# Optimization experiments

Hardware: AMD Instinct MI355X
Metric: run time of the kernel (lower is better)

The kernel has to match this reference:

```python
import jax, jax.numpy as jnp
import numpy as np

NUM_EXPERTS = 16
HIDDEN = 1024
INTERMEDIATE = 4096
TOTAL_TOKENS = 32768  # 2048 tokens per expert


def setup_inputs() -> dict:
    key = jax.random.key(0)
    k1, k2, k3 = jax.random.split(key, 3)
    hidden_states = jax.random.normal(k1, (TOTAL_TOKENS, HIDDEN), dtype=jnp.float32)
    gate_up_proj = jax.random.normal(k2, (NUM_EXPERTS, HIDDEN, 2 * INTERMEDIATE), dtype=jnp.float32)
    down_proj = jax.random.normal(k3, (NUM_EXPERTS, INTERMEDIATE, HIDDEN), dtype=jnp.float32)
    return {"hidden_states": hidden_states, "gate_up_proj": gate_up_proj, "down_proj": down_proj}


def reference(hidden_states, gate_up_proj, down_proj):
    E, H = gate_up_proj.shape[0], gate_up_proj.shape[1]
    # (E, T, H): tokens pre-grouped by expert, as in the torch module's reshape
    x = hidden_states.reshape(E, -1, H)
    # batched expert GEMM: (E,T,H) @ (E,H,2I) -> (E,T,2I)
    gate_up = jnp.einsum('eth,ehf->etf', x, gate_up_proj)
    gate, up = jnp.split(gate_up, 2, axis=-1)
    gated = up * jax.nn.silu(gate)  # SwiGLU
    # down projection: (E,T,I) @ (E,I,H) -> (E,T,H)
    out = jnp.einsum('eti,eih->eth', gated, down_proj)
    return out.reshape(-1, H)
```

## Files before the change

### kernel.cpp

```cpp
#include <hip/hip_runtime.h>
#include <hip/hip_bf16.h>
#include <cstdint>
#include <cstddef>

#define NE  16
#define HD  1024
#define ID  4096
#define TPE 2048
#define TOKENS 32768

typedef __attribute__((ext_vector_type(8))) short short8;
typedef __attribute__((ext_vector_type(4))) float f32x4;
typedef __attribute__((ext_vector_type(4))) unsigned short u16x4;
typedef __attribute__((ext_vector_type(8))) unsigned short u16x8;

static __device__ __forceinline__ unsigned short f2b(float f) {
    __bf16 h = (__bf16)f;
    return __builtin_bit_cast(unsigned short, h);
}

#define GLOAD16(gsrc, ldsbase)                                                  \
    __builtin_amdgcn_global_load_lds(                                           \
        (const __attribute__((address_space(1))) unsigned int*)(gsrc),          \
        (__attribute__((address_space(3))) unsigned int*)(ldsbase), 16, 0, 0)

#define MFMA16(a, b, c) __builtin_amdgcn_mfma_f32_16x16x32_bf16((a), (b), (c), 0, 0, 0)

__global__ void k_f2b(const float* __restrict__ src, unsigned short* __restrict__ dst, int n4)
{
    int i = blockIdx.x * blockDim.x + threadIdx.x;
    int stride = gridDim.x * blockDim.x;
    for (; i < n4; i += stride) {
        float4 v = *(const float4*)(src + (size_t)i * 4);
        u16x4 b = { f2b(v.x), f2b(v.y), f2b(v.z), f2b(v.w) };
        *(u16x4*)(dst + (size_t)i * 4) = b;
    }
}

__global__ __launch_bounds__(256) void k_transpose(const float* __restrict__ src,
                                                   unsigned short* __restrict__ dst,
                                                   int K, int N, int e0)
{
    __shared__ unsigned short LT[64][72];
    const int t  = threadIdx.x;
    const int eL = blockIdx.z;
    const float* s = src + (size_t)(e0 + eL) * K * N
                         + (size_t)(blockIdx.y * 64) * N + blockIdx.x * 64;
    unsigned short* d = dst + (size_t)eL * N * K
                            + (size_t)(blockIdx.x * 64) * K + blockIdx.y * 64;
    #pragma unroll
    for (int i = 0; i < 4; ++i) {
        int row = i * 16 + (t >> 4);
        int c4  = (t & 15) * 4;
        float4 v = *(const float4*)(s + (size_t)row * N + c4);
        LT[c4 + 0][row] = f2b(v.x);
        LT[c4 + 1][row] = f2b(v.y);
        LT[c4 + 2][row] = f2b(v.z);
        LT[c4 + 3][row] = f2b(v.w);
    }
    __syncthreads();
    #pragma unroll
    for (int i = 0; i < 2; ++i) {
        int n  = i * 32 + (t >> 3);
        int k8 = (t & 7) * 8;
        u16x8 v = *(const u16x8*)&LT[n][k8];
        *(u16x8*)(d + (size_t)n * K + k8) = v;
    }
}

__global__ __launch_bounds__(512, 2) void k_gemm1(const unsigned short* __restrict__ hsB,
                                                  const unsigned short* __restrict__ gupT,
                                                  unsigned short* __restrict__ gated,
                                                  int e0)
{
    __shared__ unsigned short As[2][256 * 64];
    __shared__ unsigned short Bs[2][256 * 64];
    const int NT = HD / 64;

    const int t    = threadIdx.x;
    const int lane = t & 63;
    const int w    = t >> 6;
    const int wr   = w >> 2;
    const int wc   = w & 3;
    const int eL   = blockIdx.z;
    const int e    = e0 + eL;
    const int n0g  = blockIdx.x * 128;
    const int m0   = blockIdx.y * 256;

    const unsigned short* gA  = hsB  + (size_t)(e * TPE + m0) * HD;
    const unsigned short* gBt = gupT + (size_t)eL * (2 * ID) * HD;

    f32x4 acc[8][4];
    #pragma unroll
    for (int i = 0; i < 8; ++i)
        #pragma unroll
        for (int j = 0; j < 4; ++j)
            acc[i][j] = f32x4{0.f, 0.f, 0.f, 0.f};

    auto STAGE = [&](int buf, int kt) {
        #pragma unroll
        for (int i = 0; i < 4; ++i) {
            int idx = i * 512 + t;
            int row = idx >> 3, sl = idx & 7;
            GLOAD16(gA + (size_t)row * HD + kt * 64 + ((sl ^ (row & 7)) << 3),
                    &As[buf][(size_t)(i * 512 + (t & ~63)) * 8]);
        }
        #pragma unroll
        for (int i = 0; i < 4; ++i) {
            int idx = i * 512 + t;
            int c = idx >> 3, sl = idx & 7;
            int g = c >> 5, j = c & 31;
            int grow = ((g & 1) ? ID : 0) + n0g + ((g >> 1) << 5) + j;
            GLOAD16(gBt + (size_t)grow * HD + kt * 64 + ((sl ^ (c & 7)) << 3),
                    &Bs[buf][(size_t)(i * 512 + (t & ~63)) * 8]);
        }
    };

    STAGE(0, 0);
    STAGE(1, 1);
    asm volatile("s_waitcnt vmcnt(8)" ::: "memory");
    __builtin_amdgcn_s_barrier();

    for (int kt = 0; kt < NT; ++kt) {
        const int cur = kt & 1;
        const unsigned short* Ab = &As[cur][0];
        const unsigned short* Bb = &Bs[cur][0];

        short8 av[8], bv[4];
        #pragma unroll
        for (int fm = 0; fm < 8; ++fm) {
            int row = wr * 128 + fm * 16 + (lane & 15);
            int sl  = (lane >> 4);
            av[fm] = *(const short8*)&Ab[row * 64 + ((sl ^ (row & 7)) << 3)];
        }
        #pragma unroll
        for (int fn = 0; fn < 4; ++fn) {
            int c  = wc * 64 + fn * 16 + (lane & 15);
            int sl = (lane >> 4);
            bv[fn] = *(const short8*)&Bb[c * 64 + ((sl ^ (c & 7)) << 3)];
        }
        __builtin_amdgcn_s_setprio(1);
        #pragma unroll
        for (int fm = 0; fm < 8; ++fm)
            #pragma unroll
            for (int fn = 0; fn < 4; ++fn)
                acc[fm][fn] = MFMA16(av[fm], bv[fn], acc[fm][fn]);
        __builtin_amdgcn_s_setprio(0);

        short8 av1[8], bv1[4];
        #pragma unroll
        for (int fm = 0; fm < 8; ++fm) {
            int row = wr * 128 + fm * 16 + (lane & 15);
            int sl  = 4 + (lane >> 4);
            av1[fm] = *(const short8*)&Ab[row * 64 + ((sl ^ (row & 7)) << 3)];
        }
        #pragma unroll
        for (int fn = 0; fn < 4; ++fn) {
            int c  = wc * 64 + fn * 16 + (lane & 15);
            int sl = 4 + (lane >> 4);
            bv1[fn] = *(const short8*)&Bb[c * 64 + ((sl ^ (c & 7)) << 3)];
        }
        asm volatile("s_waitcnt lgkmcnt(0)" ::: "memory");
        __builtin_amdgcn_sched_barrier(0);
        __builtin_amdgcn_s_barrier();
        if (kt + 2 < NT) {
            STAGE(cur, kt + 2);
            asm volatile("s_waitcnt vmcnt(8)" ::: "memory");
        } else {
            asm volatile("s_waitcnt vmcnt(0)" ::: "memory");
        }
        __builtin_amdgcn_s_barrier();
        __builtin_amdgcn_s_setprio(1);
        #pragma unroll
        for (int fm = 0; fm < 8; ++fm)
            #pragma unroll
            for (int fn = 0; fn < 4; ++fn)
                acc[fm][fn] = MFMA16(av1[fm], bv1[fn], acc[fm][fn]);
        __builtin_amdgcn_s_setprio(0);
    }

    unsigned short* g0 = gated + ((size_t)eL * TPE + m0) * ID;
    const int rq = (lane >> 4) << 2;
    const int cl = lane & 15;
    #pragma unroll
    for (int fm = 0; fm < 8; ++fm) {
        #pragma unroll
        for (int fp = 0; fp < 2; ++fp) {
            f32x4 g = acc[fm][fp];
            f32x4 u = acc[fm][fp + 2];
            #pragma unroll
            for (int r = 0; r < 4; ++r) {
                float gv  = g[r];
                float val = u[r] * gv / (1.0f + __expf(-gv));
                int row = wr * 128 + fm * 16 + rq + r;
                int col = n0g + wc * 32 + fp * 16 + cl;
                g0[(size_t)row * ID + col] = f2b(val);
            }
        }
    }
}

__global__ __launch_bounds__(512, 2) void k_gemm2(const unsigned short* __restrict__ gated,
                                                  const unsigned short* __restrict__ dwnT,
                                                  float* __restrict__ out,
                                                  int e0)
{
    __shared__ unsigned short As[2][256 * 64];
    __shared__ unsigned short Bs[2][256 * 64];
    const int NT = ID / 64;

    const int t    = threadIdx.x;
    const int lane = t & 63;
    const int w    = t >> 6;
    const int wr   = w >> 2;
    const int wc   = w & 3;
    const int eL   = blockIdx.z;
    const int e    = e0 + eL;
    const int n0   = blockIdx.x * 256;
    const int m0   = blockIdx.y * 256;

    const unsigned short* gA  = gated + ((size_t)eL * TPE + m0) * ID;
    const unsigned short* gBt = dwnT  + (size_t)eL * HD * ID;

    f32x4 acc[8][4];
    #pragma unroll
    for (int i = 0; i < 8; ++i)
        #pragma unroll
        for (int j = 0; j < 4; ++j)
            acc[i][j] = f32x4{0.f, 0.f, 0.f, 0.f};

    auto STAGE = [&](int buf, int kt) {
        #pragma unroll
        for (int i = 0; i < 4; ++i) {
            int idx = i * 512 + t;
            int row = idx >> 3, sl = idx & 7;
            GLOAD16(gA + (size_t)row * ID + kt * 64 + ((sl ^ (row & 7)) << 3),
                    &As[buf][(size_t)(i * 512 + (t & ~63)) * 8]);
        }
        #pragma unroll
        for (int i = 0; i < 4; ++i) {
            int idx = i * 512 + t;
            int c = idx >> 3, sl = idx & 7;
            GLOAD16(gBt + (size_t)(n0 + c) * ID + kt * 64 + ((sl ^ (c & 7)) << 3),
                    &Bs[buf][(size_t)(i * 512 + (t & ~63)) * 8]);
        }
    };

    STAGE(0, 0);
    STAGE(1, 1);
    asm volatile("s_waitcnt vmcnt(8)" ::: "memory");
    __builtin_amdgcn_s_barrier();

    for (int kt = 0; kt < NT; ++kt) {
        const int cur = kt & 1;
        const unsigned short* Ab = &As[cur][0];
        const unsigned short* Bb = &Bs[cur][0];

        short8 av[8], bv[4];
        #pragma unroll
        for (int fm = 0; fm < 8; ++fm) {
            int row = wr * 128 + fm * 16 + (lane & 15);
            int sl  = (lane >> 4);
            av[fm] = *(const short8*)&Ab[row * 64 + ((sl ^ (row & 7)) << 3)];
        }
        #pragma unroll
        for (int fn = 0; fn < 4; ++fn) {
            int c  = wc * 64 + fn * 16 + (lane & 15);
            int sl = (lane >> 4);
            bv[fn] = *(const short8*)&Bb[c * 64 + ((sl ^ (c & 7)) << 3)];
        }
        __builtin_amdgcn_s_setprio(1);
        #pragma unroll
        for (int fm = 0; fm < 8; ++fm)
            #pragma unroll
            for (int fn = 0; fn < 4; ++fn)
                acc[fm][fn] = MFMA16(av[fm], bv[fn], acc[fm][fn]);
        __builtin_amdgcn_s_setprio(0);

        short8 av1[8], bv1[4];
        #pragma unroll
        for (int fm = 0; fm < 8; ++fm) {
            int row = wr * 128 + fm * 16 + (lane & 15);
            int sl  = 4 + (lane >> 4);
            av1[fm] = *(const short8*)&Ab[row * 64 + ((sl ^ (row & 7)) << 3)];
        }
        #pragma unroll
        for (int fn = 0; fn < 4; ++fn) {
            int c  = wc * 64 + fn * 16 + (lane & 15);
            int sl = 4 + (lane >> 4);
            bv1[fn] = *(const short8*)&Bb[c * 64 + ((sl ^ (c & 7)) << 3)];
        }
        asm volatile("s_waitcnt lgkmcnt(0)" ::: "memory");
        __builtin_amdgcn_sched_barrier(0);
        __builtin_amdgcn_s_barrier();
        if (kt + 2 < NT) {
            STAGE(cur, kt + 2);
            asm volatile("s_waitcnt vmcnt(8)" ::: "memory");
        } else {
            asm volatile("s_waitcnt vmcnt(0)" ::: "memory");
        }
        __builtin_amdgcn_s_barrier();
        __builtin_amdgcn_s_setprio(1);
        #pragma unroll
        for (int fm = 0; fm < 8; ++fm)
            #pragma unroll
            for (int fn = 0; fn < 4; ++fn)
                acc[fm][fn] = MFMA16(av1[fm], bv1[fn], acc[fm][fn]);
        __builtin_amdgcn_s_setprio(0);
    }

    float* o0 = out + (size_t)(e * TPE + m0) * HD;
    const int rq = (lane >> 4) << 2;
    const int cl = lane & 15;
    #pragma unroll
    for (int fm = 0; fm < 8; ++fm) {
        #pragma unroll
        for (int fn = 0; fn < 4; ++fn) {
            #pragma unroll
            for (int r = 0; r < 4; ++r) {
                int row = wr * 128 + fm * 16 + rq + r;
                int col = n0 + wc * 64 + fn * 16 + cl;
                o0[(size_t)row * HD + col] = acc[fm][fn][r];
            }
        }
    }
}

extern "C" void kernel_launch(void* const* d_in, const int* in_sizes, int n_in,
                              void* d_out, int out_size, void* d_ws, size_t ws_size,
                              hipStream_t stream)
{
    (void)in_sizes; (void)n_in; (void)out_size;
    const float* hs  = (const float*)d_in[0];
    const float* gup = (const float*)d_in[1];
    const float* dwn = (const float*)d_in[2];
    float* out = (float*)d_out;

    const size_t SZ_HSB   = (size_t)TOKENS * HD * 2;
    const size_t SZ_GUPT  = (size_t)2 * ID * HD * 2;
    const size_t SZ_DWNT  = (size_t)HD * ID * 2;
    const size_t SZ_GATED = (size_t)TPE * ID * 2;
    const size_t perExp   = SZ_GUPT + SZ_DWNT + SZ_GATED;

    int G = (ws_size > SZ_HSB) ? (int)((ws_size - SZ_HSB) / perExp) : 1;
    if (G < 1) G = 1;
    if (G > NE) G = NE;

    unsigned short* hsB   = (unsigned short*)d_ws;
    unsigned short* gupT  = (unsigned short*)((char*)d_ws + SZ_HSB);
    unsigned short* dwnT  = (unsigned short*)((char*)d_ws + SZ_HSB + (size_t)G * SZ_GUPT);
    unsigned short* gated = (unsigned short*)((char*)d_ws + SZ_HSB + (size_t)G * (SZ_GUPT + SZ_DWNT));

    k_f2b<<<2048, 256, 0, stream>>>(hs, hsB, TOKENS * HD / 4);

    for (int e0 = 0; e0 < NE; e0 += G) {
        int ne = NE - e0;
        if (ne > G) ne = G;
        k_transpose<<<dim3((2 * ID) / 64, HD / 64, ne), 256, 0, stream>>>(gup, gupT, HD, 2 * ID, e0);
        k_transpose<<<dim3(HD / 64, ID / 64, ne), 256, 0, stream>>>(dwn, dwnT, ID, HD, e0);
        k_gemm1<<<dim3(ID / 128, TPE / 256, ne), 512, 0, stream>>>(hsB, gupT, gated, e0);
        k_gemm2<<<dim3(HD / 256, TPE / 256, ne), 512, 0, stream>>>(gated, dwnT, out, e0);
    }
}
```

Measured before the change: 1.173 ms.

## Interleave split global-to-LDS staging with quarter-tile MFMA phases in both GEMMs

```diff
diff --git a/kernel.cpp b/kernel.cpp
--- a/kernel.cpp
+++ b/kernel.cpp
@@ -97,87 +97,133 @@
         for (int j = 0; j < 4; ++j)
             acc[i][j] = f32x4{0.f, 0.f, 0.f, 0.f};
 
-    auto STAGE = [&](int buf, int kt) {
-        #pragma unroll
-        for (int i = 0; i < 4; ++i) {
-            int idx = i * 512 + t;
-            int row = idx >> 3, sl = idx & 7;
+    auto stageA = [&](int buf, int kt, int fmh) {
+        #pragma unroll
+        for (int i = 0; i < 2; ++i) {
+            int r0  = fmh * 64 + w * 8 + i * 128;
+            int row = r0 + (lane >> 3);
+            int sl  = lane & 7;
             GLOAD16(gA + (size_t)row * HD + kt * 64 + ((sl ^ (row & 7)) << 3),
-                    &As[buf][(size_t)(i * 512 + (t & ~63)) * 8]);
-        }
-        #pragma unroll
-        for (int i = 0; i < 4; ++i) {
-            int idx = i * 512 + t;
-            int c = idx >> 3, sl = idx & 7;
-            int g = c >> 5, j = c & 31;
-            int grow = ((g & 1) ? ID : 0) + n0g + ((g >> 1) << 5) + j;
+                    &As[buf][r0 * 64]);
+        }
+    };
+    auto stageB = [&](int buf, int kt, int half) {
+        #pragma unroll
+        for (int i = 0; i < 2; ++i) {
+            int c0 = half * 128 + w * 8 + i * 64;
+            int c  = c0 + (lane >> 3);
+            int sl = lane & 7;
+            int g  = c >> 5;
+            int grow = ((g & 1) ? ID : 0) + n0g + ((g >> 1) << 5) + (c & 31);
             GLOAD16(gBt + (size_t)grow * HD + kt * 64 + ((sl ^ (c & 7)) << 3),
-                    &Bs[buf][(size_t)(i * 512 + (t & ~63)) * 8]);
+                    &Bs[buf][c0 * 64]);
         }
     };
 
-    STAGE(0, 0);
-    STAGE(1, 1);
+    stageA(0, 0, 0);  stageB(0, 0, 0);  stageB(0, 0, 1);
+    stageA(0, 0, 1);
+    stageA(1, 1, 0);  stageB(1, 1, 0);  stageB(1, 1, 1);
     asm volatile("s_waitcnt vmcnt(8)" ::: "memory");
     __builtin_amdgcn_s_barrier();
 
     for (int kt = 0; kt < NT; ++kt) {
-        const int cur = kt & 1;
+        const int cur = kt & 1, nxt = cur ^ 1;
         const unsigned short* Ab = &As[cur][0];
         const unsigned short* Bb = &Bs[cur][0];
-
-        short8 av[8], bv[4];
-        #pragma unroll
-        for (int fm = 0; fm < 8; ++fm) {
-            int row = wr * 128 + fm * 16 + (lane & 15);
-            int sl  = (lane >> 4);
-            av[fm] = *(const short8*)&Ab[row * 64 + ((sl ^ (row & 7)) << 3)];
-        }
-        #pragma unroll
-        for (int fn = 0; fn < 4; ++fn) {
-            int c  = wc * 64 + fn * 16 + (lane & 15);
-            int sl = (lane >> 4);
-            bv[fn] = *(const short8*)&Bb[c * 64 + ((sl ^ (c & 7)) << 3)];
-        }
-        __builtin_amdgcn_s_setprio(1);
-        #pragma unroll
-        for (int fm = 0; fm < 8; ++fm)
-            #pragma unroll
-            for (int fn = 0; fn < 4; ++fn)
-                acc[fm][fn] = MFMA16(av[fm], bv[fn], acc[fm][fn]);
-        __builtin_amdgcn_s_setprio(0);
-
-        short8 av1[8], bv1[4];
-        #pragma unroll
-        for (int fm = 0; fm < 8; ++fm) {
-            int row = wr * 128 + fm * 16 + (lane & 15);
-            int sl  = 4 + (lane >> 4);
-            av1[fm] = *(const short8*)&Ab[row * 64 + ((sl ^ (row & 7)) << 3)];
-        }
-        #pragma unroll
-        for (int fn = 0; fn < 4; ++fn) {
-            int c  = wc * 64 + fn * 16 + (lane & 15);
-            int sl = 4 + (lane >> 4);
-            bv1[fn] = *(const short8*)&Bb[c * 64 + ((sl ^ (c & 7)) << 3)];
-        }
-        asm volatile("s_waitcnt lgkmcnt(0)" ::: "memory");
-        __builtin_amdgcn_sched_barrier(0);
-        __builtin_amdgcn_s_barrier();
-        if (kt + 2 < NT) {
-            STAGE(cur, kt + 2);
-            asm volatile("s_waitcnt vmcnt(8)" ::: "memory");
-        } else {
-            asm volatile("s_waitcnt vmcnt(0)" ::: "memory");
-        }
-        __builtin_amdgcn_s_barrier();
-        __builtin_amdgcn_s_setprio(1);
-        #pragma unroll
-        for (int fm = 0; fm < 8; ++fm)
-            #pragma unroll
-            for (int fn = 0; fn < 4; ++fn)
-                acc[fm][fn] = MFMA16(av1[fm], bv1[fn], acc[fm][fn]);
-        __builtin_amdgcn_s_setprio(0);
-    }
+        const int ktn  = (kt + 1 < NT) ? kt + 1 : NT - 1;
+        const int ktn2 = (kt + 2 < NT) ? kt + 2 : NT - 1;
+
+        short8 av[8], bv[8];
+
+        stageA(nxt, ktn, 1);
+        #pragma unroll
+        for (int f = 0; f < 4; ++f)
+            #pragma unroll
+            for (int ks = 0; ks < 2; ++ks) {
+                int row = wr * 128 + f * 16 + (lane & 15);
+                int sl  = ks * 4 + (lane >> 4);
+                av[f * 2 + ks] = *(const short8*)&Ab[row * 64 + ((sl ^ (row & 7)) << 3)];
+            }
+        #pragma unroll
+        for (int fn = 0; fn < 2; ++fn)
+            #pragma unroll
+            for (int ks = 0; ks < 2; ++ks) {
+                int c  = wc * 64 + fn * 16 + (lane & 15);
+                int sl = ks * 4 + (lane >> 4);
+                bv[fn * 2 + ks] = *(const short8*)&Bb[c * 64 + ((sl ^ (c & 7)) << 3)];
+            }
+        asm volatile("s_waitcnt lgkmcnt(0)" ::: "memory");
+        __builtin_amdgcn_sched_barrier(0);
+        __builtin_amdgcn_s_setprio(1);
+        #pragma unroll
+        for (int f = 0; f < 4; ++f)
+            #pragma unroll
+            for (int fn = 0; fn < 2; ++fn)
+                #pragma unroll
+                for (int ks = 0; ks < 2; ++ks)
+                    acc[f][fn] = MFMA16(av[f * 2 + ks], bv[fn * 2 + ks], acc[f][fn]);
+        __builtin_amdgcn_s_setprio(0);
+        __builtin_amdgcn_s_barrier();
+
+        stageA(cur, ktn2, 0);
+        #pragma unroll
+        for (int fn = 2; fn < 4; ++fn)
+            #pragma unroll
+            for (int ks = 0; ks < 2; ++ks) {
+                int c  = wc * 64 + fn * 16 + (lane & 15);
+                int sl = ks * 4 + (lane >> 4);
+                bv[fn * 2 + ks] = *(const short8*)&Bb[c * 64 + ((sl ^ (c & 7)) << 3)];
+            }
+        asm volatile("s_waitcnt lgkmcnt(0)" ::: "memory");
+        __builtin_amdgcn_sched_barrier(0);
+        __builtin_amdgcn_s_setprio(1);
+        #pragma unroll
+        for (int f = 0; f < 4; ++f)
+            #pragma unroll
+            for (int fn = 2; fn < 4; ++fn)
+                #pragma unroll
+                for (int ks = 0; ks < 2; ++ks)
+                    acc[f][fn] = MFMA16(av[f * 2 + ks], bv[fn * 2 + ks], acc[f][fn]);
+        __builtin_amdgcn_s_setprio(0);
+        asm volatile("s_waitcnt vmcnt(10)" ::: "memory");
+        __builtin_amdgcn_s_barrier();
+
+        stageB(cur, ktn2, 0);
+        #pragma unroll
+        for (int f = 0; f < 4; ++f)
+            #pragma unroll
+            for (int ks = 0; ks < 2; ++ks) {
+                int row = wr * 128 + 64 + f * 16 + (lane & 15);
+                int sl  = ks * 4 + (lane >> 4);
+                av[f * 2 + ks] = *(const short8*)&Ab[row * 64 + ((sl ^ (row & 7)) << 3)];
+            }
+        asm volatile("s_waitcnt lgkmcnt(0)" ::: "memory");
+        __builtin_amdgcn_sched_barrier(0);
+        __builtin_amdgcn_s_setprio(1);
+        #pragma unroll
+        for (int f = 0; f < 4; ++f)
+            #pragma unroll
+            for (int fn = 0; fn < 2; ++fn)
+                #pragma unroll
+                for (int ks = 0; ks < 2; ++ks)
+                    acc[4 + f][fn] = MFMA16(av[f * 2 + ks], bv[fn * 2 + ks], acc[4 + f][fn]);
+        __builtin_amdgcn_s_setprio(0);
+        __builtin_amdgcn_s_barrier();
+
+        stageB(cur, ktn2, 1);
+        __builtin_amdgcn_s_setprio(1);
+        #pragma unroll
+        for (int f = 0; f < 4; ++f)
+            #pragma unroll
+            for (int fn = 2; fn < 4; ++fn)
+                #pragma unroll
+                for (int ks = 0; ks < 2; ++ks)
+                    acc[4 + f][fn] = MFMA16(av[f * 2 + ks], bv[fn * 2 + ks], acc[4 + f][fn]);
+        __builtin_amdgcn_s_setprio(0);
+        asm volatile("s_waitcnt vmcnt(8)" ::: "memory");
+        __builtin_amdgcn_s_barrier();
+    }
+    asm volatile("s_waitcnt vmcnt(0)" ::: "memory");
 
     unsigned short* g0 = gated + ((size_t)eL * TPE + m0) * ID;
     const int rq = (lane >> 4) << 2;
@@ -229,85 +275,131 @@
         for (int j = 0; j < 4; ++j)
             acc[i][j] = f32x4{0.f, 0.f, 0.f, 0.f};
 
-    auto STAGE = [&](int buf, int kt) {
-        #pragma unroll
-        for (int i = 0; i < 4; ++i) {
-            int idx = i * 512 + t;
-            int row = idx >> 3, sl = idx & 7;
+    auto stageA = [&](int buf, int kt, int fmh) {
+        #pragma unroll
+        for (int i = 0; i < 2; ++i) {
+            int r0  = fmh * 64 + w * 8 + i * 128;
+            int row = r0 + (lane >> 3);
+            int sl  = lane & 7;
             GLOAD16(gA + (size_t)row * ID + kt * 64 + ((sl ^ (row & 7)) << 3),
-                    &As[buf][(size_t)(i * 512 + (t & ~63)) * 8]);
-        }
-        #pragma unroll
-        for (int i = 0; i < 4; ++i) {
-            int idx = i * 512 + t;
-            int c = idx >> 3, sl = idx & 7;
+                    &As[buf][r0 * 64]);
+        }
+    };
+    auto stageB = [&](int buf, int kt, int half) {
+        #pragma unroll
+        for (int i = 0; i < 2; ++i) {
+            int c0 = half * 128 + w * 8 + i * 64;
+            int c  = c0 + (lane >> 3);
+            int sl = lane & 7;
             GLOAD16(gBt + (size_t)(n0 + c) * ID + kt * 64 + ((sl ^ (c & 7)) << 3),
-                    &Bs[buf][(size_t)(i * 512 + (t & ~63)) * 8]);
+                    &Bs[buf][c0 * 64]);
         }
     };
 
-    STAGE(0, 0);
-    STAGE(1, 1);
+    stageA(0, 0, 0);  stageB(0, 0, 0);  stageB(0, 0, 1);
+    stageA(0, 0, 1);
+    stageA(1, 1, 0);  stageB(1, 1, 0);  stageB(1, 1, 1);
     asm volatile("s_waitcnt vmcnt(8)" ::: "memory");
     __builtin_amdgcn_s_barrier();
 
     for (int kt = 0; kt < NT; ++kt) {
-        const int cur = kt & 1;
+        const int cur = kt & 1, nxt = cur ^ 1;
         const unsigned short* Ab = &As[cur][0];
         const unsigned short* Bb = &Bs[cur][0];
-
-        short8 av[8], bv[4];
-        #pragma unroll
-        for (int fm = 0; fm < 8; ++fm) {
-            int row = wr * 128 + fm * 16 + (lane & 15);
-            int sl  = (lane >> 4);
-            av[fm] = *(const short8*)&Ab[row * 64 + ((sl ^ (row & 7)) << 3)];
-        }
-        #pragma unroll
-        for (int fn = 0; fn < 4; ++fn) {
-            int c  = wc * 64 + fn * 16 + (lane & 15);
-            int sl = (lane >> 4);
-            bv[fn] = *(const short8*)&Bb[c * 64 + ((sl ^ (c & 7)) << 3)];
-        }
-        __builtin_amdgcn_s_setprio(1);
-        #pragma unroll
-        for (int fm = 0; fm < 8; ++fm)
-            #pragma unroll
-            for (int fn = 0; fn < 4; ++fn)
-                acc[fm][fn] = MFMA16(av[fm], bv[fn], acc[fm][fn]);
-        __builtin_amdgcn_s_setprio(0);
-
-        short8 av1[8], bv1[4];
-        #pragma unroll
-        for (int fm = 0; fm < 8; ++fm) {
-            int row = wr * 128 + fm * 16 + (lane & 15);
-            int sl  = 4 + (lane >> 4);
-            av1[fm] = *(const short8*)&Ab[row * 64 + ((sl ^ (row & 7)) << 3)];
-        }
-        #pragma unroll
-        for (int fn = 0; fn < 4; ++fn) {
-            int c  = wc * 64 + fn * 16 + (lane & 15);
-            int sl = 4 + (lane >> 4);
-            bv1[fn] = *(const short8*)&Bb[c * 64 + ((sl ^ (c & 7)) << 3)];
-        }
-        asm volatile("s_waitcnt lgkmcnt(0)" ::: "memory");
-        __builtin_amdgcn_sched_barrier(0);
-        __builtin_amdgcn_s_barrier();
-        if (kt + 2 < NT) {
-            STAGE(cur, kt + 2);
-            asm volatile("s_waitcnt vmcnt(8)" ::: "memory");
-        } else {
-            asm volatile("s_waitcnt vmcnt(0)" ::: "memory");
-        }
-        __builtin_amdgcn_s_barrier();
-        __builtin_amdgcn_s_setprio(1);
-        #pragma unroll
-        for (int fm = 0; fm < 8; ++fm)
-            #pragma unroll
-            for (int fn = 0; fn < 4; ++fn)
-                acc[fm][fn] = MFMA16(av1[fm], bv1[fn], acc[fm][fn]);
-        __builtin_amdgcn_s_setprio(0);
-    }
+        const int ktn  = (kt + 1 < NT) ? kt + 1 : NT - 1;
+        const int ktn2 = (kt + 2 < NT) ? kt + 2 : NT - 1;
+
+        short8 av[8], bv[8];
+
+        stageA(nxt, ktn, 1);
+        #pragma unroll
+        for (int f = 0; f < 4; ++f)
+            #pragma unroll
+            for (int ks = 0; ks < 2; ++ks) {
+                int row = wr * 128 + f * 16 + (lane & 15);
+                int sl  = ks * 4 + (lane >> 4);
+                av[f * 2 + ks] = *(const short8*)&Ab[row * 64 + ((sl ^ (row & 7)) << 3)];
+            }
+        #pragma unroll
+        for (int fn = 0; fn < 2; ++fn)
+            #pragma unroll
+            for (int ks = 0; ks < 2; ++ks) {
+                int c  = wc * 64 + fn * 16 + (lane & 15);
+                int sl = ks * 4 + (lane >> 4);
+                bv[fn * 2 + ks] = *(const short8*)&Bb[c * 64 + ((sl ^ (c & 7)) << 3)];
+            }
+        asm volatile("s_waitcnt lgkmcnt(0)" ::: "memory");
+        __builtin_amdgcn_sched_barrier(0);
+        __builtin_amdgcn_s_setprio(1);
+        #pragma unroll
+        for (int f = 0; f < 4; ++f)
+            #pragma unroll
+            for (int fn = 0; fn < 2; ++fn)
+                #pragma unroll
+                for (int ks = 0; ks < 2; ++ks)
+                    acc[f][fn] = MFMA16(av[f * 2 + ks], bv[fn * 2 + ks], acc[f][fn]);
+        __builtin_amdgcn_s_setprio(0);
+        __builtin_amdgcn_s_barrier();
+
+        stageA(cur, ktn2, 0);
+        #pragma unroll
+        for (int fn = 2; fn < 4; ++fn)
+            #pragma unroll
+            for (int ks = 0; ks < 2; ++ks) {
+                int c  = wc * 64 + fn * 16 + (lane & 15);
+                int sl = ks * 4 + (lane >> 4);
+                bv[fn * 2 + ks] = *(const short8*)&Bb[c * 64 + ((sl ^ (c & 7)) << 3)];
+            }
+        asm volatile("s_waitcnt lgkmcnt(0)" ::: "memory");
+        __builtin_amdgcn_sched_barrier(0);
+        __builtin_amdgcn_s_setprio(1);
+        #pragma unroll
+        for (int f = 0; f < 4; ++f)
+            #pragma unroll
+            for (int fn = 2; fn < 4; ++fn)
+                #pragma unroll
+                for (int ks = 0; ks < 2; ++ks)
+                    acc[f][fn] = MFMA16(av[f * 2 + ks], bv[fn * 2 + ks], acc[f][fn]);
+        __builtin_amdgcn_s_setprio(0);
+        asm volatile("s_waitcnt vmcnt(10)" ::: "memory");
+        __builtin_amdgcn_s_barrier();
+
+        stageB(cur, ktn2, 0);
+        #pragma unroll
+        for (int f = 0; f < 4; ++f)
+            #pragma unroll
+            for (int ks = 0; ks < 2; ++ks) {
+                int row = wr * 128 + 64 + f * 16 + (lane & 15);
+                int sl  = ks * 4 + (lane >> 4);
+                av[f * 2 + ks] = *(const short8*)&Ab[row * 64 + ((sl ^ (row & 7)) << 3)];
+            }
+        asm volatile("s_waitcnt lgkmcnt(0)" ::: "memory");
+        __builtin_amdgcn_sched_barrier(0);
+        __builtin_amdgcn_s_setprio(1);
+        #pragma unroll
+        for (int f = 0; f < 4; ++f)
+            #pragma unroll
+            for (int fn = 0; fn < 2; ++fn)
+                #pragma unroll
+                for (int ks = 0; ks < 2; ++ks)
+                    acc[4 + f][fn] = MFMA16(av[f * 2 + ks], bv[fn * 2 + ks], acc[4 + f][fn]);
+        __builtin_amdgcn_s_setprio(0);
+        __builtin_amdgcn_s_barrier();
+
+        stageB(cur, ktn2, 1);
+        __builtin_amdgcn_s_setprio(1);
+        #pragma unroll
+        for (int f = 0; f < 4; ++f)
+            #pragma unroll
+            for (int fn = 2; fn < 4; ++fn)
+                #pragma unroll
+                for (int ks = 0; ks < 2; ++ks)
+                    acc[4 + f][fn] = MFMA16(av[f * 2 + ks], bv[fn * 2 + ks], acc[4 + f][fn]);
+        __builtin_amdgcn_s_setprio(0);
+        asm volatile("s_waitcnt vmcnt(8)" ::: "memory");
+        __builtin_amdgcn_s_barrier();
+    }
+    asm volatile("s_waitcnt vmcnt(0)" ::: "memory");
 
     float* o0 = out + (size_t)(e * TPE + m0) * HD;
     const int rq = (lane >> 4) << 2;
```

Result: slower. 1.372 ms (+16.9%).

## Software-pipeline LDS fragment reads across k-substeps in both expert GEMMs

Applied to the files above, without the earlier changes.

```diff
diff --git a/kernel.cpp b/kernel.cpp
--- a/kernel.cpp
+++ b/kernel.cpp
@@ -110,9 +110,29 @@
             int idx = i * 512 + t;
             int c = idx >> 3, sl = idx & 7;
             int g = c >> 5, j = c & 31;
-            int grow = ((g & 1) ? ID : 0) + n0g + ((g >> 1) << 5) + j;
+            int grow = ((g & 1) ? ID : 0) + n0g + ((g >> 1) << 5) + (c & 31);
+            (void)j;
             GLOAD16(gBt + (size_t)grow * HD + kt * 64 + ((sl ^ (c & 7)) << 3),
                     &Bs[buf][(size_t)(i * 512 + (t & ~63)) * 8]);
+        }
+    };
+
+    short8 avP[8], bvP[4], avQ[8], bvQ[4];
+
+    auto READ_A = [&](const unsigned short* Ab, int ks, short8* av) {
+        #pragma unroll
+        for (int f = 0; f < 8; ++f) {
+            int row = wr * 128 + f * 16 + (lane & 15);
+            int sl  = ks * 4 + (lane >> 4);
+            av[f] = *(const short8*)&Ab[row * 64 + ((sl ^ (row & 7)) << 3)];
+        }
+    };
+    auto READ_B = [&](const unsigned short* Bb, int ks, short8* bv) {
+        #pragma unroll
+        for (int fn = 0; fn < 4; ++fn) {
+            int c  = wc * 64 + fn * 16 + (lane & 15);
+            int sl = ks * 4 + (lane >> 4);
+            bv[fn] = *(const short8*)&Bb[c * 64 + ((sl ^ (c & 7)) << 3)];
         }
     };
 
@@ -120,64 +140,45 @@
     STAGE(1, 1);
     asm volatile("s_waitcnt vmcnt(8)" ::: "memory");
     __builtin_amdgcn_s_barrier();
+    READ_A(&As[0][0], 0, avP);  READ_B(&Bs[0][0], 0, bvP);
 
     for (int kt = 0; kt < NT; ++kt) {
         const int cur = kt & 1;
-        const unsigned short* Ab = &As[cur][0];
-        const unsigned short* Bb = &Bs[cur][0];
-
-        short8 av[8], bv[4];
-        #pragma unroll
-        for (int fm = 0; fm < 8; ++fm) {
-            int row = wr * 128 + fm * 16 + (lane & 15);
-            int sl  = (lane >> 4);
-            av[fm] = *(const short8*)&Ab[row * 64 + ((sl ^ (row & 7)) << 3)];
-        }
-        #pragma unroll
-        for (int fn = 0; fn < 4; ++fn) {
-            int c  = wc * 64 + fn * 16 + (lane & 15);
-            int sl = (lane >> 4);
-            bv[fn] = *(const short8*)&Bb[c * 64 + ((sl ^ (c & 7)) << 3)];
-        }
+        const unsigned short* Ab  = &As[cur][0];
+        const unsigned short* Bb  = &Bs[cur][0];
+        const unsigned short* Abn = &As[cur ^ 1][0];
+        const unsigned short* Bbn = &Bs[cur ^ 1][0];
+        const int ktn2 = (kt + 2 < NT) ? kt + 2 : NT - 1;
+
+        READ_A(Ab, 1, avQ);  READ_B(Bb, 1, bvQ);
+        asm volatile("s_waitcnt lgkmcnt(12)" ::: "memory");
+        __builtin_amdgcn_sched_barrier(0);
         __builtin_amdgcn_s_setprio(1);
         #pragma unroll
-        for (int fm = 0; fm < 8; ++fm)
+        for (int f = 0; f < 8; ++f)
             #pragma unroll
             for (int fn = 0; fn < 4; ++fn)
-                acc[fm][fn] = MFMA16(av[fm], bv[fn], acc[fm][fn]);
+                acc[f][fn] = MFMA16(avP[f], bvP[fn], acc[f][fn]);
         __builtin_amdgcn_s_setprio(0);
 
-        short8 av1[8], bv1[4];
-        #pragma unroll
-        for (int fm = 0; fm < 8; ++fm) {
-            int row = wr * 128 + fm * 16 + (lane & 15);
-            int sl  = 4 + (lane >> 4);
-            av1[fm] = *(const short8*)&Ab[row * 64 + ((sl ^ (row & 7)) << 3)];
-        }
-        #pragma unroll
-        for (int fn = 0; fn < 4; ++fn) {
-            int c  = wc * 64 + fn * 16 + (lane & 15);
-            int sl = 4 + (lane >> 4);
-            bv1[fn] = *(const short8*)&Bb[c * 64 + ((sl ^ (c & 7)) << 3)];
-        }
         asm volatile("s_waitcnt lgkmcnt(0)" ::: "memory");
+        __builtin_amdgcn_s_barrier();
+        STAGE(cur, ktn2);
+        asm volatile("s_waitcnt vmcnt(8)" ::: "memory");
+        __builtin_amdgcn_s_barrier();
         __builtin_amdgcn_sched_barrier(0);
-        __builtin_amdgcn_s_barrier();
-        if (kt + 2 < NT) {
-            STAGE(cur, kt + 2);
-            asm volatile("s_waitcnt vmcnt(8)" ::: "memory");
-        } else {
-            asm volatile("s_waitcnt vmcnt(0)" ::: "memory");
-        }
-        __builtin_amdgcn_s_barrier();
+
+        READ_A(Abn, 0, avP);  READ_B(Bbn, 0, bvP);
+
         __builtin_amdgcn_s_setprio(1);
         #pragma unroll
-        for (int fm = 0; fm < 8; ++fm)
+        for (int f = 0; f < 8; ++f)
             #pragma unroll
             for (int fn = 0; fn < 4; ++fn)
-                acc[fm][fn] = MFMA16(av1[fm], bv1[fn], acc[fm][fn]);
+                acc[f][fn] = MFMA16(avQ[f], bvQ[fn], acc[f][fn]);
         __builtin_amdgcn_s_setprio(0);
     }
+    asm volatile("s_waitcnt vmcnt(0)" ::: "memory");
 
     unsigned short* g0 = gated + ((size_t)eL * TPE + m0) * ID;
     const int rq = (lane >> 4) << 2;
@@ -246,68 +247,68 @@
         }
     };
 
+    short8 avP[8], bvP[4], avQ[8], bvQ[4];
+
+    auto READ_A = [&](const unsigned short* Ab, int ks, short8* av) {
+        #pragma unroll
+        for (int f = 0; f < 8; ++f) {
+            int row = wr * 128 + f * 16 + (lane & 15);
+            int sl  = ks * 4 + (lane >> 4);
+            av[f] = *(const short8*)&Ab[row * 64 + ((sl ^ (row & 7)) << 3)];
+        }
+    };
+    auto READ_B = [&](const unsigned short* Bb, int ks, short8* bv) {
+        #pragma unroll
+        for (int fn = 0; fn < 4; ++fn) {
+            int c  = wc * 64 + fn * 16 + (lane & 15);
+            int sl = ks * 4 + (lane >> 4);
+            bv[fn] = *(const short8*)&Bb[c * 64 + ((sl ^ (c & 7)) << 3)];
+        }
+    };
+
     STAGE(0, 0);
     STAGE(1, 1);
     asm volatile("s_waitcnt vmcnt(8)" ::: "memory");
     __builtin_amdgcn_s_barrier();
+    READ_A(&As[0][0], 0, avP);  READ_B(&Bs[0][0], 0, bvP);
 
     for (int kt = 0; kt < NT; ++kt) {
         const int cur = kt & 1;
-        const unsigned short* Ab = &As[cur][0];
-        const unsigned short* Bb = &Bs[cur][0];
-
-        short8 av[8], bv[4];
-        #pragma unroll
-        for (int fm = 0; fm < 8; ++fm) {
-            int row = wr * 128 + fm * 16 + (lane & 15);
-            int sl  = (lane >> 4);
-            av[fm] = *(const short8*)&Ab[row * 64 + ((sl ^ (row & 7)) << 3)];
-        }
-        #pragma unroll
-        for (int fn = 0; fn < 4; ++fn) {
-            int c  = wc * 64 + fn * 16 + (lane & 15);
-            int sl = (lane >> 4);
-            bv[fn] = *(const short8*)&Bb[c * 64 + ((sl ^ (c & 7)) << 3)];
-        }
+        const unsigned short* Ab  = &As[cur][0];
+        const unsigned short* Bb  = &Bs[cur][0];
+        const unsigned short* Abn = &As[cur ^ 1][0];
+        const unsigned short* Bbn = &Bs[cur ^ 1][0];
+        const int ktn2 = (kt + 2 < NT) ? kt + 2 : NT - 1;
+
+        READ_A(Ab, 1, avQ);  READ_B(Bb, 1, bvQ);
+        asm volatile("s_waitcnt lgkmcnt(12)" ::: "memory");
+        __builtin_amdgcn_sched_barrier(0);
         __builtin_amdgcn_s_setprio(1);
         #pragma unroll
-        for (int fm = 0; fm < 8; ++fm)
+        for (int f = 0; f < 8; ++f)
             #pragma unroll
             for (int fn = 0; fn < 4; ++fn)
-                acc[fm][fn] = MFMA16(av[fm], bv[fn], acc[fm][fn]);
+                acc[f][fn] = MFMA16(avP[f], bvP[fn], acc[f][fn]);
         __builtin_amdgcn_s_setprio(0);
 
-        short8 av1[8], bv1[4];
-        #pragma unroll
-        for (int fm = 0; fm < 8; ++fm) {
-            int row = wr * 128 + fm * 16 + (lane & 15);
-            int sl  = 4 + (lane >> 4);
-            av1[fm] = *(const short8*)&Ab[row * 64 + ((sl ^ (row & 7)) << 3)];
-        }
-        #pragma unroll
-        for (int fn = 0; fn < 4; ++fn) {
-            int c  = wc * 64 + fn * 16 + (lane & 15);
-            int sl = 4 + (lane >> 4);
-            bv1[fn] = *(const short8*)&Bb[c * 64 + ((sl ^ (c & 7)) << 3)];
-        }
         asm volatile("s_waitcnt lgkmcnt(0)" ::: "memory");
+        __builtin_amdgcn_s_barrier();
+        STAGE(cur, ktn2);
+        asm volatile("s_waitcnt vmcnt(8)" ::: "memory");
+        __builtin_amdgcn_s_barrier();
         __builtin_amdgcn_sched_barrier(0);
-        __builtin_amdgcn_s_barrier();
-        if (kt + 2 < NT) {
-            STAGE(cur, kt + 2);
-            asm volatile("s_waitcnt vmcnt(8)" ::: "memory");
-        } else {
-            asm volatile("s_waitcnt vmcnt(0)" ::: "memory");
-        }
-        __builtin_amdgcn_s_barrier();
+
+        READ_A(Abn, 0, avP);  READ_B(Bbn, 0, bvP);
+
         __builtin_amdgcn_s_setprio(1);
         #pragma unroll
-        for (int fm = 0; fm < 8; ++fm)
+        for (int f = 0; f < 8; ++f)
             #pragma unroll
             for (int fn = 0; fn < 4; ++fn)
-                acc[fm][fn] = MFMA16(av1[fm], bv1[fn], acc[fm][fn]);
+                acc[f][fn] = MFMA16(avQ[f], bvQ[fn], acc[f][fn]);
         __builtin_amdgcn_s_setprio(0);
     }
+    asm volatile("s_waitcnt vmcnt(0)" ::: "memory");
 
     float* o0 = out + (size_t)(e * TPE + m0) * HD;
     const int rq = (lane >> 4) << 2;
```

After: 1.284 ms. 1.09x slower.
